# Kernel optimization log

Measured on AMD Instinct MI355X. Metric: run time of the kernel, lower is better.

## Reference

```python
import jax, jax.numpy as jnp
import numpy as np

IN_DIM = 64

def setup_inputs() -> dict:
    key = jax.random.key(0)
    ks = jax.random.split(key, 9)
    B, C, H, W = 4, IN_DIM, 256, 256
    scale = 1.0 / np.sqrt(3 * C)  # conv fan-in init scale
    return {
        'rgb': jax.random.normal(ks[0], (B, C, H, W), dtype=jnp.float32),
        'hsv': jax.random.normal(ks[1], (B, C, H, W), dtype=jnp.float32),
        'lab': jax.random.normal(ks[2], (B, C, H, W), dtype=jnp.float32),
        'Wq': jax.random.normal(ks[3], (C, 3 * C), dtype=jnp.float32) * scale,
        'bq': jax.random.normal(ks[4], (C,), dtype=jnp.float32) * scale,
        'Wk': jax.random.normal(ks[5], (C, 3 * C), dtype=jnp.float32) * scale,
        'bk': jax.random.normal(ks[6], (C,), dtype=jnp.float32) * scale,
        'Wv': jax.random.normal(ks[7], (C, 3 * C), dtype=jnp.float32) * scale,
        'bv': jax.random.normal(ks[8], (C,), dtype=jnp.float32) * scale,
    }

def _proj(x, W, b):
    # 1x1 conv: [B,3C,H,W] x [C,3C] -> [B,C,H,W]
    return jnp.einsum('oc,bchw->bohw', W, x) + b[None, :, None, None]

def reference(rgb, hsv, lab, Wq, bq, Wk, bk, Wv, bv):
    B, C, H, W = rgb.shape
    combined = jnp.concatenate([rgb, hsv, lab], axis=1)  # [B,3C,H,W]
    q = _proj(combined, Wq, bq).reshape(B, C, H * W)     # [B,C,N]
    k = _proj(combined, Wk, bk).reshape(B, C, H * W)     # [B,C,N]
    v = _proj(combined, Wv, bv).reshape(B, C, H * W)     # [B,C,N]
    energy = jnp.einsum('bcn,bdn->bcd', q, k) * (C ** -0.5)  # [B,C,C]
    attention = jax.nn.softmax(energy, axis=-1)
    out = jnp.einsum('bcd,bdn->bcn', attention, v)           # [B,C,N]
    return out.reshape(B, C, H, W)
```

## Files before the change

kernel.cpp:

```cpp
#include <hip/hip_runtime.h>
#include <cstddef>


#define NPIX 65536

typedef _Float16 half4_t __attribute__((ext_vector_type(4)));
typedef _Float16 half8_t __attribute__((ext_vector_type(8)));
typedef float f32x4_t __attribute__((ext_vector_type(4)));

__global__ void k0_zero(float* __restrict__ p, int n) {
  int i = blockIdx.x * 256 + threadIdx.x;
  if (i < n) p[i] = 0.0f;
}

__global__ __launch_bounds__(768, 3) void k1_gram(
    const float* __restrict__ rgb, const float* __restrict__ hsv, const float* __restrict__ lab,
    float* __restrict__ G, float* __restrict__ S, float* __restrict__ part, int use_part) {
  __shared__ alignas(16) unsigned char smem[24576];
  _Float16* lds = (_Float16*)smem;
  float* slds = (float*)smem;

  const int t = threadIdx.x;
  const int lane = t & 63;
  const int w = t >> 6;
  const int wi = w & 1;
  const int wj = w >> 1;
  const int b = blockIdx.y;
  const int n0 = blockIdx.x * 1024;

  const int row = t >> 2;
  const int cq = (t & 3) << 4;
  const float* srcs[3] = {rgb, hsv, lab};
  const float* gp = srcs[row >> 6] + (size_t)(b * 64 + (row & 63)) * NPIX + n0 + cq;

  f32x4_t acc[6][2];
  const f32x4_t zero4 = {0.0f, 0.0f, 0.0f, 0.0f};
#pragma unroll
  for (int a = 0; a < 6; ++a)
#pragma unroll
    for (int j = 0; j < 2; ++j) acc[a][j] = zero4;
  float s_acc = 0.0f;

  const int sw = (row & 7) << 3;
  const int rbase = row * 64;

  float4 A0, A1, A2, A3, B0, B1, B2, B3;
  auto loadA = [&](int cc) {
    const float* p = gp + cc * 64;
    A0 = *(const float4*)(p + 0); A1 = *(const float4*)(p + 4);
    A2 = *(const float4*)(p + 8); A3 = *(const float4*)(p + 12);
  };
  auto loadB = [&](int cc) {
    const float* p = gp + cc * 64;
    B0 = *(const float4*)(p + 0); B1 = *(const float4*)(p + 4);
    B2 = *(const float4*)(p + 8); B3 = *(const float4*)(p + 12);
  };
  auto writeLDS = [&](float4 r0, float4 r1, float4 r2, float4 r3) {
    s_acc += (r0.x + r0.y + r0.z + r0.w) + (r1.x + r1.y + r1.z + r1.w) +
             (r2.x + r2.y + r2.z + r2.w) + (r3.x + r3.y + r3.z + r3.w);
    half4_t h;
    h.x = (_Float16)r0.x; h.y = (_Float16)r0.y; h.z = (_Float16)r0.z; h.w = (_Float16)r0.w;
    *(half4_t*)(lds + rbase + ((cq + 0) ^ sw)) = h;
    h.x = (_Float16)r1.x; h.y = (_Float16)r1.y; h.z = (_Float16)r1.z; h.w = (_Float16)r1.w;
    *(half4_t*)(lds + rbase + ((cq + 4) ^ sw)) = h;
    h.x = (_Float16)r2.x; h.y = (_Float16)r2.y; h.z = (_Float16)r2.z; h.w = (_Float16)r2.w;
    *(half4_t*)(lds + rbase + ((cq + 8) ^ sw)) = h;
    h.x = (_Float16)r3.x; h.y = (_Float16)r3.y; h.z = (_Float16)r3.z; h.w = (_Float16)r3.w;
    *(half4_t*)(lds + rbase + ((cq + 12) ^ sw)) = h;
  };
  auto compute = [&]() {
#pragma unroll
    for (int ks = 0; ks < 2; ++ks) {
      const int kc = ks * 32 + 8 * (lane >> 4);
      half8_t fA[6], fB[2];
#pragma unroll
      for (int a = 0; a < 6; ++a) {
        int rA = wi * 96 + a * 16 + (lane & 15);
        fA[a] = *(const half8_t*)(lds + rA * 64 + (kc ^ ((rA & 7) << 3)));
      }
#pragma unroll
      for (int j = 0; j < 2; ++j) {
        int rB = (wj * 2 + j) * 16 + (lane & 15);
        fB[j] = *(const half8_t*)(lds + rB * 64 + (kc ^ ((rB & 7) << 3)));
      }
#pragma unroll
      for (int a = 0; a < 6; ++a)
#pragma unroll
        for (int j = 0; j < 2; ++j)
          acc[a][j] = __builtin_amdgcn_mfma_f32_16x16x32_f16(fA[a], fB[j], acc[a][j], 0, 0, 0);
    }
  };

  loadA(0);
  loadB(1);
  for (int cc = 0; cc < 16; cc += 2) {
    writeLDS(A0, A1, A2, A3);
    __syncthreads();
    if (cc + 2 < 16) loadA(cc + 2);
    compute();
    __syncthreads();
    writeLDS(B0, B1, B2, B3);
    __syncthreads();
    if (cc + 3 < 16) loadB(cc + 3);
    compute();
    __syncthreads();
  }

  if (use_part) {
    float* pb = part + (size_t)(b * 64 + blockIdx.x) * 37056;
#pragma unroll
    for (int a = 0; a < 6; ++a)
#pragma unroll
      for (int j = 0; j < 2; ++j) {
        int tt = (wi * 6 + a) * 12 + (wj * 2 + j);
        *(f32x4_t*)(pb + tt * 256 + lane * 4) = acc[a][j];
      }
  } else {
    float* Gb = G + b * 36864;
#pragma unroll
    for (int a = 0; a < 6; ++a)
#pragma unroll
      for (int j = 0; j < 2; ++j) {
        int I = wi * 6 + a, J = wj * 2 + j;
#pragma unroll
        for (int r = 0; r < 4; ++r) {
          int gr = I * 16 + ((lane >> 4) << 2) + r;
          int gc = J * 16 + (lane & 15);
          atomicAdd(Gb + gr * 192 + gc, acc[a][j][r]);
        }
      }
  }

  slds[t] = s_acc;
  __syncthreads();
  if (t < 192) {
    float s = (slds[t * 4] + slds[t * 4 + 1]) + (slds[t * 4 + 2] + slds[t * 4 + 3]);
    if (use_part)
      part[(size_t)(b * 64 + blockIdx.x) * 37056 + 36864 + t] = s;
    else
      atomicAdd(S + b * 192 + t, s);
  }
}

__global__ void k1r_reduce(const float* __restrict__ part, float* __restrict__ G,
                           float* __restrict__ S) {
  int idx = blockIdx.x * 256 + threadIdx.x;
  if (idx >= 4 * 37056) return;
  int b = idx / 37056;
  int flat = idx % 37056;
  const float* base = part + (size_t)b * 64 * 37056 + flat;
  float v0 = 0.f, v1 = 0.f, v2 = 0.f, v3 = 0.f;
#pragma unroll
  for (int q = 0; q < 64; q += 4) {
    v0 += base[(size_t)(q + 0) * 37056];
    v1 += base[(size_t)(q + 1) * 37056];
    v2 += base[(size_t)(q + 2) * 37056];
    v3 += base[(size_t)(q + 3) * 37056];
  }
  float v = (v0 + v1) + (v2 + v3);
  if (flat < 36864) {
    int tt = flat >> 8;
    int I = tt / 12, J = tt % 12;
    int r = flat & 255;
    int lane = r >> 2, rg = r & 3;
    int row = I * 16 + ((lane >> 4) << 2) + rg;
    int col = J * 16 + (lane & 15);
    G[b * 36864 + row * 192 + col] = v;
  } else {
    S[b * 192 + (flat - 36864)] = v;
  }
}

__global__ __launch_bounds__(256) void k2_small(
    const float* __restrict__ G, const float* __restrict__ S,
    const float* __restrict__ Wq, const float* __restrict__ bq,
    const float* __restrict__ Wk, const float* __restrict__ bk,
    const float* __restrict__ Wv, const float* __restrict__ bv,
    _Float16* __restrict__ Mh, float* __restrict__ c0w) {
  const int b = blockIdx.y;
  const int cbase = blockIdx.x * 8;
  const int t = threadIdx.x;
  __shared__ float T1[192 * 9];
  __shared__ float el[64 * 8];
  __shared__ float sq[8];
  __shared__ float sk[64];
  const float* Gb = G + b * 36864;
  const float* Sb = S + b * 192;

  if (t < 8) {
    float a = 0.f;
    const float* wq = Wq + (cbase + t) * 192;
    for (int i = 0; i < 192; ++i) a = fmaf(wq[i], Sb[i], a);
    sq[t] = a;
  } else if (t < 72) {
    int d = t - 8;
    float a = 0.f;
    const float* wk = Wk + d * 192;
    for (int j = 0; j < 192; ++j) a = fmaf(wk[j], Sb[j], a);
    sk[d] = a;
  }
  for (int e = t; e < 1536; e += 256) {
    int j = e % 192, cp = e / 192;
    const float* wq = Wq + (cbase + cp) * 192;
    float a = 0.f;
    for (int i = 0; i < 192; ++i) a = fmaf(wq[i], Gb[i * 192 + j], a);
    T1[j * 9 + cp] = a;
  }
  __syncthreads();
  for (int e = t; e < 512; e += 256) {
    int cp = e & 7, d = e >> 3;
    const float* wk = Wk + d * 192;
    float a = 0.f;
    for (int j = 0; j < 192; ++j) a = fmaf(T1[j * 9 + cp], wk[j], a);
    float bqc = bq[cbase + cp], bkd = bk[d];
    a += bqc * sk[d] + bkd * sq[cp] + 65536.0f * bqc * bkd;
    el[d * 8 + cp] = a * 0.125f;
  }
  __syncthreads();
  if (t < 8) {
    float mx = -3.0e38f;
    for (int d = 0; d < 64; ++d) mx = fmaxf(mx, el[d * 8 + t]);
    float sum = 0.f;
    for (int d = 0; d < 64; ++d) {
      float pv = expf(el[d * 8 + t] - mx);
      el[d * 8 + t] = pv;
      sum += pv;
    }
    float inv = 1.0f / sum;
    for (int d = 0; d < 64; ++d) el[d * 8 + t] *= inv;
  }
  __syncthreads();
  for (int e = t; e < 1536; e += 256) {
    int i = e % 192, cp = e / 192;
    int c = cbase + cp;
    float a = 0.f;
    for (int d = 0; d < 64; ++d) a = fmaf(el[d * 8 + cp], Wv[d * 192 + i], a);
    Mh[(size_t)b * 12288 + c * 192 + (i ^ ((c & 7) << 3))] = (_Float16)a;
  }
  if (t < 8) {
    float a = 0.f;
    for (int d = 0; d < 64; ++d) a = fmaf(el[d * 8 + t], bv[d], a);
    c0w[b * 64 + cbase + t] = a;
  }
}

__global__ __launch_bounds__(256, 3) void k3_out(
    const float* __restrict__ rgb, const float* __restrict__ hsv, const float* __restrict__ lab,
    const _Float16* __restrict__ Mh, const float* __restrict__ c0w, float* __restrict__ out) {
  __shared__ alignas(16) _Float16 lds_m[12288];
  __shared__ alignas(16) _Float16 lds_x[8192];
  __shared__ float c0l[64];
  const int t = threadIdx.x;
  const int lane = t & 63;
  const int w = t >> 6;
  const int b = blockIdx.y;
  const int nblk = blockIdx.x * 256;

  {
    const float4* msrc = (const float4*)(Mh + (size_t)b * 12288);
    float4* mdst = (float4*)lds_m;
#pragma unroll
    for (int k = 0; k < 6; ++k) mdst[t + 256 * k] = msrc[t + 256 * k];
    if (t < 64) c0l[t] = c0w[b * 64 + t];
  }

  const int xi = t & 31;
  const int ng = t >> 5;
  const float* srcs[3] = {rgb, hsv, lab};

  f32x4_t acc[4][4];
  const f32x4_t zero4 = {0.0f, 0.0f, 0.0f, 0.0f};
#pragma unroll
  for (int i = 0; i < 4; ++i)
#pragma unroll
    for (int j = 0; j < 4; ++j) acc[i][j] = zero4;

  float4 xr[8];
  auto xload = [&](int kc) {
    int ig = kc * 32 + xi;
    const float* p = srcs[ig >> 6] + (size_t)(b * 64 + (ig & 63)) * NPIX + nblk + ng * 32;
#pragma unroll
    for (int f = 0; f < 8; ++f) xr[f] = *(const float4*)(p + f * 4);
  };
  auto xwrite = [&]() {
#pragma unroll
    for (int f = 0; f < 8; ++f) {
      int n = ng * 32 + f * 4;
      lds_x[(n + 0) * 32 + (xi ^ 0)]  = (_Float16)xr[f].x;
      lds_x[(n + 1) * 32 + (xi ^ 8)]  = (_Float16)xr[f].y;
      lds_x[(n + 2) * 32 + (xi ^ 16)] = (_Float16)xr[f].z;
      lds_x[(n + 3) * 32 + (xi ^ 24)] = (_Float16)xr[f].w;
    }
  };

  const int g = lane >> 4;
  const int l15 = lane & 15;

  xload(0);
  for (int kc = 0; kc < 6; ++kc) {
    xwrite();
    __syncthreads();
    if (kc + 1 < 6) xload(kc + 1);
    half8_t fx[4], fm[4];
#pragma unroll
    for (int nt = 0; nt < 4; ++nt) {
      int n = w * 64 + nt * 16 + l15;
      fx[nt] = *(const half8_t*)(lds_x + n * 32 + ((8 * g) ^ ((n & 3) << 3)));
    }
#pragma unroll
    for (int ct = 0; ct < 4; ++ct) {
      int c = ct * 16 + l15;
      fm[ct] = *(const half8_t*)(lds_m + c * 192 + ((kc * 32 + 8 * g) ^ ((c & 7) << 3)));
    }
#pragma unroll
    for (int nt = 0; nt < 4; ++nt)
#pragma unroll
      for (int ct = 0; ct < 4; ++ct)
        acc[nt][ct] = __builtin_amdgcn_mfma_f32_16x16x32_f16(fx[nt], fm[ct], acc[nt][ct], 0, 0, 0);
    __syncthreads();
  }

#pragma unroll
  for (int ct = 0; ct < 4; ++ct) {
    int c = ct * 16 + l15;
    float c0v = c0l[c];
#pragma unroll
    for (int nt = 0; nt < 4; ++nt) {
      int n = nblk + w * 64 + nt * 16 + 4 * g;
      float4 o;
      o.x = acc[nt][ct][0] + c0v;
      o.y = acc[nt][ct][1] + c0v;
      o.z = acc[nt][ct][2] + c0v;
      o.w = acc[nt][ct][3] + c0v;
      *(float4*)(out + (size_t)(b * 64 + c) * NPIX + n) = o;
    }
  }
}

extern "C" void kernel_launch(void* const* d_in, const int* in_sizes, int n_in,
                              void* d_out, int out_size, void* d_ws, size_t ws_size,
                              hipStream_t stream) {
  const float* rgb = (const float*)d_in[0];
  const float* hsv = (const float*)d_in[1];
  const float* lab = (const float*)d_in[2];
  const float* Wq = (const float*)d_in[3];
  const float* bq = (const float*)d_in[4];
  const float* Wk = (const float*)d_in[5];
  const float* bk = (const float*)d_in[6];
  const float* Wv = (const float*)d_in[7];
  const float* bv = (const float*)d_in[8];
  float* out = (float*)d_out;
  float* ws = (float*)d_ws;

  float* G = ws;
  float* S = ws + 147456;
  _Float16* Mh = (_Float16*)(ws + 148224);
  float* c0w = ws + 172800;
  float* part = ws + 173056;
  const int use_part =
      (ws_size >= (size_t)(173056 + 9486336) * sizeof(float)) ? 1 : 0;

  if (!use_part)
    k0_zero<<<dim3(579), dim3(256), 0, stream>>>(ws, 148224);
  k1_gram<<<dim3(64, 4), dim3(768), 0, stream>>>(rgb, hsv, lab, G, S, part, use_part);
  if (use_part)
    k1r_reduce<<<dim3(579), dim3(256), 0, stream>>>(part, G, S);
  k2_small<<<dim3(8, 4), dim3(256), 0, stream>>>(G, S, Wq, bq, Wk, bk, Wv, bv, Mh, c0w);
  k3_out<<<dim3(256, 4), dim3(256), 0, stream>>>(rgb, hsv, lab, Mh, c0w, out);
}
```

Measured before the change: 147.9 us.

## Split Gram kernel into twice as many blocks with double-buffered LDS

The Gram-matrix kernel now uses 512 pixels per block instead of 1024, doubling the grid to 128x4 blocks. It double-buffers the fp16 LDS tile so each chunk needs only one barrier, and remaps the 12 waves to a 4x3 MFMA tile per wave. Partial results go to a larger partial buffer (or are merged with atomics when workspace is short) and are then reduced over 128 partials. The goal is better occupancy and latency hiding on the 256 CUs. The cost is twice the partial-sum traffic in the reduce kernel and more LDS per block.

```diff
diff --git a/kernel.cpp b/kernel.cpp
--- a/kernel.cpp
+++ b/kernel.cpp
@@ -13,115 +13,115 @@
   if (i < n) p[i] = 0.0f;
 }
 
-__global__ __launch_bounds__(768, 3) void k1_gram(
+__global__ __launch_bounds__(768, 6) void k1_gram(
     const float* __restrict__ rgb, const float* __restrict__ hsv, const float* __restrict__ lab,
-    float* __restrict__ G, float* __restrict__ S, float* __restrict__ part, int use_part) {
-  __shared__ alignas(16) unsigned char smem[24576];
-  _Float16* lds = (_Float16*)smem;
-  float* slds = (float*)smem;
+    float* __restrict__ G, float* __restrict__ S, float* __restrict__ part, int mode) {
+  __shared__ alignas(16) _Float16 lds2[2][12288];
+  float* slds = (float*)&lds2[0][0];
 
   const int t = threadIdx.x;
   const int lane = t & 63;
   const int w = t >> 6;
-  const int wi = w & 1;
-  const int wj = w >> 1;
+  const int wi = w >> 2;
+  const int wj = w & 3;
   const int b = blockIdx.y;
-  const int n0 = blockIdx.x * 1024;
+  const int bx = blockIdx.x;
+  const int n0 = bx * 512;
 
   const int row = t >> 2;
   const int cq = (t & 3) << 4;
   const float* srcs[3] = {rgb, hsv, lab};
   const float* gp = srcs[row >> 6] + (size_t)(b * 64 + (row & 63)) * NPIX + n0 + cq;
 
-  f32x4_t acc[6][2];
+  f32x4_t acc[4][3];
   const f32x4_t zero4 = {0.0f, 0.0f, 0.0f, 0.0f};
 #pragma unroll
-  for (int a = 0; a < 6; ++a)
-#pragma unroll
-    for (int j = 0; j < 2; ++j) acc[a][j] = zero4;
+  for (int a = 0; a < 4; ++a)
+#pragma unroll
+    for (int j = 0; j < 3; ++j) acc[a][j] = zero4;
   float s_acc = 0.0f;
 
   const int sw = (row & 7) << 3;
   const int rbase = row * 64;
 
-  float4 A0, A1, A2, A3, B0, B1, B2, B3;
-  auto loadA = [&](int cc) {
+  float4 R0, R1, R2, R3;
+  auto loadR = [&](int cc) {
     const float* p = gp + cc * 64;
-    A0 = *(const float4*)(p + 0); A1 = *(const float4*)(p + 4);
-    A2 = *(const float4*)(p + 8); A3 = *(const float4*)(p + 12);
-  };
-  auto loadB = [&](int cc) {
-    const float* p = gp + cc * 64;
-    B0 = *(const float4*)(p + 0); B1 = *(const float4*)(p + 4);
-    B2 = *(const float4*)(p + 8); B3 = *(const float4*)(p + 12);
-  };
-  auto writeLDS = [&](float4 r0, float4 r1, float4 r2, float4 r3) {
-    s_acc += (r0.x + r0.y + r0.z + r0.w) + (r1.x + r1.y + r1.z + r1.w) +
-             (r2.x + r2.y + r2.z + r2.w) + (r3.x + r3.y + r3.z + r3.w);
+    R0 = *(const float4*)(p + 0); R1 = *(const float4*)(p + 4);
+    R2 = *(const float4*)(p + 8); R3 = *(const float4*)(p + 12);
+  };
+  auto writeL = [&](_Float16* buf) {
+    s_acc += (R0.x + R0.y + R0.z + R0.w) + (R1.x + R1.y + R1.z + R1.w) +
+             (R2.x + R2.y + R2.z + R2.w) + (R3.x + R3.y + R3.z + R3.w);
     half4_t h;
-    h.x = (_Float16)r0.x; h.y = (_Float16)r0.y; h.z = (_Float16)r0.z; h.w = (_Float16)r0.w;
-    *(half4_t*)(lds + rbase + ((cq + 0) ^ sw)) = h;
-    h.x = (_Float16)r1.x; h.y = (_Float16)r1.y; h.z = (_Float16)r1.z; h.w = (_Float16)r1.w;
-    *(half4_t*)(lds + rbase + ((cq + 4) ^ sw)) = h;
-    h.x = (_Float16)r2.x; h.y = (_Float16)r2.y; h.z = (_Float16)r2.z; h.w = (_Float16)r2.w;
-    *(half4_t*)(lds + rbase + ((cq + 8) ^ sw)) = h;
-    h.x = (_Float16)r3.x; h.y = (_Float16)r3.y; h.z = (_Float16)r3.z; h.w = (_Float16)r3.w;
-    *(half4_t*)(lds + rbase + ((cq + 12) ^ sw)) = h;
-  };
-  auto compute = [&]() {
+    h.x = (_Float16)R0.x; h.y = (_Float16)R0.y; h.z = (_Float16)R0.z; h.w = (_Float16)R0.w;
+    *(half4_t*)(buf + rbase + ((cq + 0) ^ sw)) = h;
+    h.x = (_Float16)R1.x; h.y = (_Float16)R1.y; h.z = (_Float16)R1.z; h.w = (_Float16)R1.w;
+    *(half4_t*)(buf + rbase + ((cq + 4) ^ sw)) = h;
+    h.x = (_Float16)R2.x; h.y = (_Float16)R2.y; h.z = (_Float16)R2.z; h.w = (_Float16)R2.w;
+    *(half4_t*)(buf + rbase + ((cq + 8) ^ sw)) = h;
+    h.x = (_Float16)R3.x; h.y = (_Float16)R3.y; h.z = (_Float16)R3.z; h.w = (_Float16)R3.w;
+    *(half4_t*)(buf + rbase + ((cq + 12) ^ sw)) = h;
+  };
+  auto compute = [&](const _Float16* buf) {
 #pragma unroll
     for (int ks = 0; ks < 2; ++ks) {
       const int kc = ks * 32 + 8 * (lane >> 4);
-      half8_t fA[6], fB[2];
-#pragma unroll
-      for (int a = 0; a < 6; ++a) {
-        int rA = wi * 96 + a * 16 + (lane & 15);
-        fA[a] = *(const half8_t*)(lds + rA * 64 + (kc ^ ((rA & 7) << 3)));
-      }
-#pragma unroll
-      for (int j = 0; j < 2; ++j) {
-        int rB = (wj * 2 + j) * 16 + (lane & 15);
-        fB[j] = *(const half8_t*)(lds + rB * 64 + (kc ^ ((rB & 7) << 3)));
-      }
-#pragma unroll
-      for (int a = 0; a < 6; ++a)
-#pragma unroll
-        for (int j = 0; j < 2; ++j)
+      half8_t fA[4], fB[3];
+#pragma unroll
+      for (int a = 0; a < 4; ++a) {
+        int rA = wi * 64 + a * 16 + (lane & 15);
+        fA[a] = *(const half8_t*)(buf + rA * 64 + (kc ^ ((rA & 7) << 3)));
+      }
+#pragma unroll
+      for (int j = 0; j < 3; ++j) {
+        int rB = wj * 48 + j * 16 + (lane & 15);
+        fB[j] = *(const half8_t*)(buf + rB * 64 + (kc ^ ((rB & 7) << 3)));
+      }
+#pragma unroll
+      for (int a = 0; a < 4; ++a)
+#pragma unroll
+        for (int j = 0; j < 3; ++j)
           acc[a][j] = __builtin_amdgcn_mfma_f32_16x16x32_f16(fA[a], fB[j], acc[a][j], 0, 0, 0);
     }
   };
 
-  loadA(0);
-  loadB(1);
-  for (int cc = 0; cc < 16; cc += 2) {
-    writeLDS(A0, A1, A2, A3);
+  loadR(0);
+  for (int cc = 0; cc < 8; ++cc) {
+    writeL(&lds2[cc & 1][0]);
     __syncthreads();
-    if (cc + 2 < 16) loadA(cc + 2);
-    compute();
-    __syncthreads();
-    writeLDS(B0, B1, B2, B3);
-    __syncthreads();
-    if (cc + 3 < 16) loadB(cc + 3);
-    compute();
-    __syncthreads();
-  }
-
-  if (use_part) {
-    float* pb = part + (size_t)(b * 64 + blockIdx.x) * 37056;
-#pragma unroll
-    for (int a = 0; a < 6; ++a)
-#pragma unroll
-      for (int j = 0; j < 2; ++j) {
-        int tt = (wi * 6 + a) * 12 + (wj * 2 + j);
+    if (cc + 1 < 8) loadR(cc + 1);
+    compute(&lds2[cc & 1][0]);
+  }
+  __syncthreads();
+
+  if (mode == 2) {
+    float* pb = part + (size_t)(b * 128 + bx) * 37056;
+#pragma unroll
+    for (int a = 0; a < 4; ++a)
+#pragma unroll
+      for (int j = 0; j < 3; ++j) {
+        int tt = (wi * 4 + a) * 12 + (wj * 3 + j);
         *(f32x4_t*)(pb + tt * 256 + lane * 4) = acc[a][j];
+      }
+  } else if (mode == 1) {
+    float* pb = part + (size_t)(b * 64 + (bx >> 1)) * 37056;
+#pragma unroll
+    for (int a = 0; a < 4; ++a)
+#pragma unroll
+      for (int j = 0; j < 3; ++j) {
+        int tt = (wi * 4 + a) * 12 + (wj * 3 + j);
+#pragma unroll
+        for (int r = 0; r < 4; ++r)
+          atomicAdd(pb + tt * 256 + lane * 4 + r, acc[a][j][r]);
       }
   } else {
     float* Gb = G + b * 36864;
 #pragma unroll
-    for (int a = 0; a < 6; ++a)
-#pragma unroll
-      for (int j = 0; j < 2; ++j) {
-        int I = wi * 6 + a, J = wj * 2 + j;
+    for (int a = 0; a < 4; ++a)
+#pragma unroll
+      for (int j = 0; j < 3; ++j) {
+        int I = wi * 4 + a, J = wj * 3 + j;
 #pragma unroll
         for (int r = 0; r < 4; ++r) {
           int gr = I * 16 + ((lane >> 4) << 2) + r;
@@ -135,23 +135,24 @@
   __syncthreads();
   if (t < 192) {
     float s = (slds[t * 4] + slds[t * 4 + 1]) + (slds[t * 4 + 2] + slds[t * 4 + 3]);
-    if (use_part)
-      part[(size_t)(b * 64 + blockIdx.x) * 37056 + 36864 + t] = s;
+    if (mode == 2)
+      part[(size_t)(b * 128 + bx) * 37056 + 36864 + t] = s;
+    else if (mode == 1)
+      atomicAdd(part + (size_t)(b * 64 + (bx >> 1)) * 37056 + 36864 + t, s);
     else
       atomicAdd(S + b * 192 + t, s);
   }
 }
 
 __global__ void k1r_reduce(const float* __restrict__ part, float* __restrict__ G,
-                           float* __restrict__ S) {
+                           float* __restrict__ S, int P) {
   int idx = blockIdx.x * 256 + threadIdx.x;
   if (idx >= 4 * 37056) return;
   int b = idx / 37056;
   int flat = idx % 37056;
-  const float* base = part + (size_t)b * 64 * 37056 + flat;
+  const float* base = part + (size_t)b * P * 37056 + flat;
   float v0 = 0.f, v1 = 0.f, v2 = 0.f, v3 = 0.f;
-#pragma unroll
-  for (int q = 0; q < 64; q += 4) {
+  for (int q = 0; q < P; q += 4) {
     v0 += base[(size_t)(q + 0) * 37056];
     v1 += base[(size_t)(q + 1) * 37056];
     v2 += base[(size_t)(q + 2) * 37056];
@@ -357,14 +358,18 @@
   _Float16* Mh = (_Float16*)(ws + 148224);
   float* c0w = ws + 172800;
   float* part = ws + 173056;
-  const int use_part =
-      (ws_size >= (size_t)(173056 + 9486336) * sizeof(float)) ? 1 : 0;
-
-  if (!use_part)
+  const size_t need2 = (size_t)(173056 + 512 * 37056) * 4;
+  const size_t need1 = (size_t)(173056 + 256 * 37056) * 4;
+  const int mode = ws_size >= need2 ? 2 : (ws_size >= need1 ? 1 : 0);
+
+  if (mode == 1)
+    k0_zero<<<dim3(37056), dim3(256), 0, stream>>>(part, 256 * 37056);
+  else if (mode == 0)
     k0_zero<<<dim3(579), dim3(256), 0, stream>>>(ws, 148224);
-  k1_gram<<<dim3(64, 4), dim3(768), 0, stream>>>(rgb, hsv, lab, G, S, part, use_part);
-  if (use_part)
-    k1r_reduce<<<dim3(579), dim3(256), 0, stream>>>(part, G, S);
+
+  k1_gram<<<dim3(128, 4), dim3(768), 0, stream>>>(rgb, hsv, lab, G, S, part, mode);
+  if (mode)
+    k1r_reduce<<<dim3(579), dim3(256), 0, stream>>>(part, G, S, mode == 2 ? 128 : 64);
   k2_small<<<dim3(8, 4), dim3(256), 0, stream>>>(G, S, Wq, bq, Wk, bk, Wv, bv, Mh, c0w);
   k3_out<<<dim3(256, 4), dim3(256), 0, stream>>>(rgb, hsv, lab, Mh, c0w, out);
 }
```

Result: slower. 287.0 us (+94.0%).
